# Performance work log

Hardware: AMD Instinct MI355X
Metric: run time of the kernel (lower is better)

The kernel has to match this reference:

```python
import jax, jax.numpy as jnp
import numpy as np

N_NODES = 50000
N_EDGES = 800000
N_GRAPHS = 64


def setup_inputs() -> dict:
    key = jax.random.key(0)
    ks = jax.random.split(key, 13)
    x = jax.random.normal(ks[0], (N_NODES, 1), dtype=jnp.float32)
    edge_index = jax.random.randint(ks[1], (2, N_EDGES), 0, N_NODES)
    batch = jnp.sort(jax.random.randint(ks[2], (N_NODES,), 0, N_GRAPHS))
    def glorot(k, shape):
        fan_in, fan_out = shape
        s = jnp.sqrt(6.0 / (fan_in + fan_out))
        return jax.random.uniform(k, shape, jnp.float32, -s, s)
    W1 = glorot(ks[3], (1, 128));    b1 = jnp.zeros((128,), jnp.float32)
    W2 = glorot(ks[4], (128, 128));  b2 = jnp.zeros((128,), jnp.float32)
    W3 = glorot(ks[5], (128, 256));  b3 = jnp.zeros((256,), jnp.float32)
    Wf1 = glorot(ks[6], (256, 128)); bf1 = jnp.zeros((128,), jnp.float32)
    Wf2 = glorot(ks[7], (128, 10));  bf2 = jnp.zeros((10,), jnp.float32)
    return {"x": x, "edge_index": edge_index, "batch": batch,
            "W1": W1, "b1": b1, "W2": W2, "b2": b2, "W3": W3, "b3": b3,
            "Wf1": Wf1, "bf1": bf1, "Wf2": Wf2, "bf2": bf2}


def _gcn_conv(x, W, b, src, dst, n_nodes):
    # PyG GCNConv: h = X W; out = D^{-1/2} (A + I) D^{-1/2} h + b
    h = x @ W                                  # [N, F_out]
    loop = jnp.arange(n_nodes)
    s = jnp.concatenate([src, loop])           # sources incl. self-loops
    d = jnp.concatenate([dst, loop])           # targets incl. self-loops
    deg = jax.ops.segment_sum(jnp.ones_like(d, h.dtype), d, num_segments=n_nodes)
    dis = jax.lax.rsqrt(jnp.maximum(deg, 1e-12))  # deg >= 1 due to self-loops
    norm = dis[s] * dis[d]                     # [E+N]
    out = jax.ops.segment_sum(h[s] * norm[:, None], d, num_segments=n_nodes)
    return out + b


def reference(x, edge_index, batch, W1, b1, W2, b2, W3, b3, Wf1, bf1, Wf2, bf2):
    src, dst = edge_index[0], edge_index[1]
    n = x.shape[0]
    h = jax.nn.relu(_gcn_conv(x, W1, b1, src, dst, n))
    h = jax.nn.relu(_gcn_conv(h, W2, b2, src, dst, n))
    h = jax.nn.relu(_gcn_conv(h, W3, b3, src, dst, n))   # [N, 256]
    g = jax.ops.segment_max(h, batch, num_segments=N_GRAPHS)  # global_max_pool [G, 256]
    g = jax.nn.relu(g @ Wf1 + bf1)
    # F.dropout with training=self.training: identity in eval mode
    g = g @ Wf2 + bf2
    return jax.nn.relu(g)                       # [G, 10]
```

## Files before the change

### kernel.cpp

```cpp
#include <hip/hip_runtime.h>
#include <hip/hip_bf16.h>

#define N_GRAPHS 64

typedef float f32x4 __attribute__((ext_vector_type(4)));
typedef short bf16x8 __attribute__((ext_vector_type(8)));

__device__ inline unsigned short f2bf(float f) {
    unsigned int u = __float_as_uint(f);
    u = u + 0x7fffu + ((u >> 16) & 1u);
    return (unsigned short)(u >> 16);
}
__device__ inline float bf2f(unsigned short h) {
    return __uint_as_float(((unsigned int)h) << 16);
}

__global__ void k_deg(const int* __restrict__ dst, int E, int* __restrict__ deg) {
    int i = blockIdx.x * blockDim.x + threadIdx.x;
    if (i < E) atomicAdd(&deg[dst[i]], 1);
}

__global__ void k_dis_bsum(const int* __restrict__ deg, const float* __restrict__ x,
                           float* __restrict__ dis, float* __restrict__ xp,
                           int* __restrict__ bsum, int N) {
    int i = blockIdx.x * 256 + threadIdx.x;
    int dv = (i < N) ? deg[i] : 0;
    if (i < N) {
        float d = rsqrtf((float)(dv + 1));
        dis[i] = d;
        xp[i]  = d * x[i];
    }
    int v = dv;
#pragma unroll
    for (int o = 1; o < 64; o <<= 1) v += __shfl_xor(v, o);
    __shared__ int ws4[4];
    if ((threadIdx.x & 63) == 0) ws4[threadIdx.x >> 6] = v;
    __syncthreads();
    if (threadIdx.x == 0) bsum[blockIdx.x] = ws4[0] + ws4[1] + ws4[2] + ws4[3];
}

__device__ inline int block_scan_inc(int v, int* wsum) {
    int lane = threadIdx.x & 63, w = threadIdx.x >> 6;
    int iv = v;
#pragma unroll
    for (int o = 1; o < 64; o <<= 1) {
        int t = __shfl_up(iv, o);
        if (lane >= o) iv += t;
    }
    if (lane == 63) wsum[w] = iv;
    __syncthreads();
    int add = 0;
    for (int k = 0; k < w; ++k) add += wsum[k];
    return iv + add;
}

__global__ void k_scan_sums(const int* __restrict__ bsum, int nb, int* __restrict__ boff) {
    __shared__ int wsum[4];
    int tid = threadIdx.x;
    int v = (tid < nb) ? bsum[tid] : 0;
    int inc = block_scan_inc(v, wsum);
    if (tid < nb) boff[tid] = inc - v;
}

__global__ void k_scan_apply(const int* __restrict__ deg, const int* __restrict__ boff,
                             int* __restrict__ row_ptr, int N) {
    __shared__ int wsum[4];
    int b = blockIdx.x, i = b * 256 + threadIdx.x;
    int v = (i < N) ? deg[i] : 0;
    int inc = block_scan_inc(v, wsum) + boff[b];
    if (i < N) {
        row_ptr[i] = inc - v;
        if (i == N - 1) row_ptr[N] = inc;
    }
}

__global__ void k_scatter(const int* __restrict__ src, const int* __restrict__ dst, int E,
                          const int* __restrict__ row_ptr, int* __restrict__ fill,
                          int* __restrict__ csr_src) {
    int e = blockIdx.x * blockDim.x + threadIdx.x;
    if (e < E) {
        int d = dst[e];
        int pos = row_ptr[d] + atomicAdd(&fill[d], 1);
        csr_src[pos] = src[e];
    }
}

__global__ void k_agg_scalar(const float* __restrict__ xp, const float* __restrict__ dis,
                             const int* __restrict__ row_ptr, const int* __restrict__ csr,
                             float2* __restrict__ td2, int N) {
    int d = blockIdx.x * blockDim.x + threadIdx.x;
    if (d >= N) return;
    float acc = xp[d];
    int e0 = row_ptr[d], e1 = row_ptr[d + 1];
    int e = e0;
    for (; e + 8 <= e1; e += 8) {
        int s0 = csr[e],     s1 = csr[e + 1], s2 = csr[e + 2], s3 = csr[e + 3];
        int s4 = csr[e + 4], s5 = csr[e + 5], s6 = csr[e + 6], s7 = csr[e + 7];
        acc += ((xp[s0] + xp[s1]) + (xp[s2] + xp[s3]))
             + ((xp[s4] + xp[s5]) + (xp[s6] + xp[s7]));
    }
    for (; e < e1; ++e) acc += xp[csr[e]];
    float dd = dis[d];
    td2[d] = make_float2(dd * acc, dd);
}

__global__ void k_h1agg(const float2* __restrict__ td2,
                        const float4* __restrict__ W1f4, const float4* __restrict__ b1f4,
                        const int* __restrict__ row_ptr, const int* __restrict__ csr,
                        float4* __restrict__ out4, int N) {
    int node = blockIdx.x * 8 + (threadIdx.x >> 5);
    int lane = threadIdx.x & 31;
    if (node >= N) return;
    const float4 w1 = W1f4[lane];
    const float4 bv = b1f4[lane];
    float2 sv = td2[node];
    float dd = sv.y;
    float a0 = dd * fmaxf(fmaf(sv.x, w1.x, bv.x), 0.f);
    float a1 = dd * fmaxf(fmaf(sv.x, w1.y, bv.y), 0.f);
    float a2 = dd * fmaxf(fmaf(sv.x, w1.z, bv.z), 0.f);
    float a3 = dd * fmaxf(fmaf(sv.x, w1.w, bv.w), 0.f);
    int e0 = row_ptr[node], e1 = row_ptr[node + 1];
    int e = e0;
    for (; e + 8 <= e1; e += 8) {
        int s0 = csr[e],     s1 = csr[e + 1], s2 = csr[e + 2], s3 = csr[e + 3];
        int s4 = csr[e + 4], s5 = csr[e + 5], s6 = csr[e + 6], s7 = csr[e + 7];
        float2 v0 = td2[s0], v1 = td2[s1], v2 = td2[s2], v3 = td2[s3];
        float2 v4 = td2[s4], v5 = td2[s5], v6 = td2[s6], v7 = td2[s7];
        a0 += ((v0.y * fmaxf(fmaf(v0.x, w1.x, bv.x), 0.f)
              + v1.y * fmaxf(fmaf(v1.x, w1.x, bv.x), 0.f))
             + (v2.y * fmaxf(fmaf(v2.x, w1.x, bv.x), 0.f)
              + v3.y * fmaxf(fmaf(v3.x, w1.x, bv.x), 0.f)))
            + ((v4.y * fmaxf(fmaf(v4.x, w1.x, bv.x), 0.f)
              + v5.y * fmaxf(fmaf(v5.x, w1.x, bv.x), 0.f))
             + (v6.y * fmaxf(fmaf(v6.x, w1.x, bv.x), 0.f)
              + v7.y * fmaxf(fmaf(v7.x, w1.x, bv.x), 0.f)));
        a1 += ((v0.y * fmaxf(fmaf(v0.x, w1.y, bv.y), 0.f)
              + v1.y * fmaxf(fmaf(v1.x, w1.y, bv.y), 0.f))
             + (v2.y * fmaxf(fmaf(v2.x, w1.y, bv.y), 0.f)
              + v3.y * fmaxf(fmaf(v3.x, w1.y, bv.y), 0.f)))
            + ((v4.y * fmaxf(fmaf(v4.x, w1.y, bv.y), 0.f)
              + v5.y * fmaxf(fmaf(v5.x, w1.y, bv.y), 0.f))
             + (v6.y * fmaxf(fmaf(v6.x, w1.y, bv.y), 0.f)
              + v7.y * fmaxf(fmaf(v7.x, w1.y, bv.y), 0.f)));
        a2 += ((v0.y * fmaxf(fmaf(v0.x, w1.z, bv.z), 0.f)
              + v1.y * fmaxf(fmaf(v1.x, w1.z, bv.z), 0.f))
             + (v2.y * fmaxf(fmaf(v2.x, w1.z, bv.z), 0.f)
              + v3.y * fmaxf(fmaf(v3.x, w1.z, bv.z), 0.f)))
            + ((v4.y * fmaxf(fmaf(v4.x, w1.z, bv.z), 0.f)
              + v5.y * fmaxf(fmaf(v5.x, w1.z, bv.z), 0.f))
             + (v6.y * fmaxf(fmaf(v6.x, w1.z, bv.z), 0.f)
              + v7.y * fmaxf(fmaf(v7.x, w1.z, bv.z), 0.f)));
        a3 += ((v0.y * fmaxf(fmaf(v0.x, w1.w, bv.w), 0.f)
              + v1.y * fmaxf(fmaf(v1.x, w1.w, bv.w), 0.f))
             + (v2.y * fmaxf(fmaf(v2.x, w1.w, bv.w), 0.f)
              + v3.y * fmaxf(fmaf(v3.x, w1.w, bv.w), 0.f)))
            + ((v4.y * fmaxf(fmaf(v4.x, w1.w, bv.w), 0.f)
              + v5.y * fmaxf(fmaf(v5.x, w1.w, bv.w), 0.f))
             + (v6.y * fmaxf(fmaf(v6.x, w1.w, bv.w), 0.f)
              + v7.y * fmaxf(fmaf(v7.x, w1.w, bv.w), 0.f)));
    }
    for (; e < e1; ++e) {
        float2 v = td2[csr[e]];
        a0 += v.y * fmaxf(fmaf(v.x, w1.x, bv.x), 0.f);
        a1 += v.y * fmaxf(fmaf(v.x, w1.y, bv.y), 0.f);
        a2 += v.y * fmaxf(fmaf(v.x, w1.z, bv.z), 0.f);
        a3 += v.y * fmaxf(fmaf(v.x, w1.w, bv.w), 0.f);
    }
    out4[(size_t)node * 32 + lane] = make_float4(a0 * dd, a1 * dd, a2 * dd, a3 * dd);
}

__global__ void k_agg128(const float4* __restrict__ hp4, const float* __restrict__ dis,
                         const int* __restrict__ row_ptr, const int* __restrict__ csr,
                         float4* __restrict__ out4, int N) {
    int node = blockIdx.x * 8 + (threadIdx.x >> 5);
    int lane = threadIdx.x & 31;
    if (node >= N) return;
    float4 self = hp4[(size_t)node * 32 + lane];
    float a0 = self.x, a1 = self.y, a2 = self.z, a3 = self.w;
    int e0 = row_ptr[node], e1 = row_ptr[node + 1];
    int e = e0;
    for (; e + 8 <= e1; e += 8) {
        int s0 = csr[e],     s1 = csr[e + 1], s2 = csr[e + 2], s3 = csr[e + 3];
        int s4 = csr[e + 4], s5 = csr[e + 5], s6 = csr[e + 6], s7 = csr[e + 7];
        float4 v0 = hp4[(size_t)s0 * 32 + lane];
        float4 v1 = hp4[(size_t)s1 * 32 + lane];
        float4 v2 = hp4[(size_t)s2 * 32 + lane];
        float4 v3 = hp4[(size_t)s3 * 32 + lane];
        float4 v4 = hp4[(size_t)s4 * 32 + lane];
        float4 v5 = hp4[(size_t)s5 * 32 + lane];
        float4 v6 = hp4[(size_t)s6 * 32 + lane];
        float4 v7 = hp4[(size_t)s7 * 32 + lane];
        a0 += ((v0.x + v1.x) + (v2.x + v3.x)) + ((v4.x + v5.x) + (v6.x + v7.x));
        a1 += ((v0.y + v1.y) + (v2.y + v3.y)) + ((v4.y + v5.y) + (v6.y + v7.y));
        a2 += ((v0.z + v1.z) + (v2.z + v3.z)) + ((v4.z + v5.z) + (v6.z + v7.z));
        a3 += ((v0.w + v1.w) + (v2.w + v3.w)) + ((v4.w + v5.w) + (v6.w + v7.w));
    }
    for (; e < e1; ++e) {
        int s = csr[e];
        float4 v = hp4[(size_t)s * 32 + lane];
        a0 += v.x; a1 += v.y; a2 += v.z; a3 += v.w;
    }
    float d = dis[node];
    out4[(size_t)node * 32 + lane] = make_float4(a0 * d, a1 * d, a2 * d, a3 * d);
}

__global__ void k_wpack(const float* __restrict__ W, int K, int F,
                        unsigned short* __restrict__ WpH,
                        unsigned short* __restrict__ WpL) {
    int idx = blockIdx.x * 256 + threadIdx.x;
    if (idx >= K * F) return;
    int k = idx / F, col = idx - k * F;
    float v = W[idx];
    unsigned short h = f2bf(v);
    unsigned short l = f2bf(v - bf2f(h));
    int o = ((k >> 3) * F + col) * 8 + (k & 7);
    WpH[o] = h; WpL[o] = l;
}

template<int FOUT, bool SCALE, bool FUSE_MAX>
__global__ __launch_bounds__(256, 3) void k_gemm_mfma(
        const float* __restrict__ A,
        const unsigned short* __restrict__ WpH, const unsigned short* __restrict__ WpL,
        const float* __restrict__ b, const float* __restrict__ dis,
        float* __restrict__ outp, const int* __restrict__ batch,
        unsigned int* __restrict__ gmax, int N) {
    __shared__ __align__(16) unsigned short ApH[4 * 4 * 16 * 8];
    __shared__ __align__(16) unsigned short ApL[4 * 4 * 16 * 8];
    __shared__ __align__(16) unsigned short WlH[4 * 128 * 8];
    __shared__ __align__(16) unsigned short WlL[4 * 128 * 8];
    const int tid  = threadIdx.x;
    const int lane = tid & 63;
    const int w    = tid >> 6;
    const int n0   = blockIdx.x * 64;
    const int jh   = blockIdx.y;

    f32x4 acc[8];
#pragma unroll
    for (int ct = 0; ct < 8; ++ct) acc[ct] = (f32x4){0.f, 0.f, 0.f, 0.f};

    for (int kc = 0; kc < 128; kc += 32) {
#pragma unroll
        for (int it = 0; it < 2; ++it) {
            int q = tid + it * 256;
            int kg = q >> 7, cq = q & 127;
            int src = ((kc >> 3) + kg) * FOUT + jh * 128 + cq;
            ((f32x4*)WlH)[q] = ((const f32x4*)WpH)[src];
            ((f32x4*)WlL)[q] = ((const f32x4*)WpL)[src];
        }
#pragma unroll
        for (int it = 0; it < 2; ++it) {
            int idx = tid + it * 256;
            int node = idx >> 3, k4 = idx & 7;
            int gn = n0 + node;
            float4 a = (gn < N)
                ? *reinterpret_cast<const float4*>(A + (size_t)gn * 128 + kc + k4 * 4)
                : make_float4(0.f, 0.f, 0.f, 0.f);
            unsigned short h0 = f2bf(a.x), h1 = f2bf(a.y), h2 = f2bf(a.z), h3 = f2bf(a.w);
            unsigned short l0 = f2bf(a.x - bf2f(h0)), l1 = f2bf(a.y - bf2f(h1));
            unsigned short l2 = f2bf(a.z - bf2f(h2)), l3 = f2bf(a.w - bf2f(h3));
            int kg = k4 >> 1, e0 = (k4 & 1) * 4;
            int base = (((node >> 4) * 4 + kg) * 16 + (node & 15)) * 8 + e0;
            *reinterpret_cast<ushort4*>(&ApH[base]) = make_ushort4(h0, h1, h2, h3);
            *reinterpret_cast<ushort4*>(&ApL[base]) = make_ushort4(l0, l1, l2, l3);
        }
        __syncthreads();

        int aidx = (w * 4 + (lane >> 4)) * 16 + (lane & 15);
        bf16x8 aH = ((const bf16x8*)ApH)[aidx];
        bf16x8 aL = ((const bf16x8*)ApL)[aidx];
#pragma unroll
        for (int ct = 0; ct < 8; ++ct) {
            int bidx = (lane >> 4) * 128 + ct * 16 + (lane & 15);
            bf16x8 bH = ((const bf16x8*)WlH)[bidx];
            bf16x8 bL = ((const bf16x8*)WlL)[bidx];
            acc[ct] = __builtin_amdgcn_mfma_f32_16x16x32_bf16(aL, bL, acc[ct], 0, 0, 0);
            acc[ct] = __builtin_amdgcn_mfma_f32_16x16x32_bf16(aL, bH, acc[ct], 0, 0, 0);
            acc[ct] = __builtin_amdgcn_mfma_f32_16x16x32_bf16(aH, bL, acc[ct], 0, 0, 0);
            acc[ct] = __builtin_amdgcn_mfma_f32_16x16x32_bf16(aH, bH, acc[ct], 0, 0, 0);
        }
        __syncthreads();
    }

    const int cl = lane & 15;
    const int r0 = (lane >> 4) * 4;
    float bb[8];
#pragma unroll
    for (int ct = 0; ct < 8; ++ct) bb[ct] = b[jh * 128 + ct * 16 + cl];

    if (!FUSE_MAX) {
#pragma unroll
        for (int r = 0; r < 4; ++r) {
            int node = n0 + w * 16 + r0 + r;
            if (node < N) {
                float dsc = SCALE ? dis[node] : 1.f;
                float* op = outp + (size_t)node * FOUT + jh * 128 + cl;
#pragma unroll
                for (int ct = 0; ct < 8; ++ct) {
                    float v = fmaxf(acc[ct][r] + bb[ct], 0.f);
                    op[ct * 16] = SCALE ? v * dsc : v;
                }
            }
        }
    } else {
        int nbm[4];
#pragma unroll
        for (int r = 0; r < 4; ++r) {
            int node = n0 + w * 16 + r0 + r;
            nbm[r] = (node < N) ? batch[node] : -1;
        }
        int gfirst = batch[n0];
        int glast  = batch[min(n0 + 63, N - 1)];
        for (int gb = gfirst; gb <= glast; ++gb) {
#pragma unroll
            for (int ct = 0; ct < 8; ++ct) {
                float m = 0.f;
#pragma unroll
                for (int r = 0; r < 4; ++r) {
                    float v = fmaxf(acc[ct][r] + bb[ct], 0.f);
                    if (nbm[r] == gb) m = fmaxf(m, v);
                }
                m = fmaxf(m, __shfl_xor(m, 16));
                m = fmaxf(m, __shfl_xor(m, 32));
                if ((lane >> 4) == 0)
                    atomicMax(&gmax[gb * 256 + jh * 128 + ct * 16 + cl],
                              __float_as_uint(m));
            }
        }
    }
}

__global__ void k_mlp(const float* __restrict__ g, const float* __restrict__ Wf1,
                      const float* __restrict__ bf1, const float* __restrict__ Wf2,
                      const float* __restrict__ bf2, float* __restrict__ out) {
    __shared__ float gr[256];
    __shared__ float g1s[128];
    const int gid = blockIdx.x;
    const int tid = threadIdx.x;
    gr[tid] = g[gid * 256 + tid];
    gr[tid + 128] = g[gid * 256 + 128 + tid];
    __syncthreads();
    float acc = bf1[tid];
    for (int k = 0; k < 256; ++k)
        acc = fmaf(gr[k], Wf1[k * 128 + tid], acc);
    g1s[tid] = fmaxf(acc, 0.f);
    __syncthreads();
    if (tid < 10) {
        float a = bf2[tid];
        for (int k = 0; k < 128; ++k)
            a = fmaf(g1s[k], Wf2[k * 10 + tid], a);
        out[gid * 10 + tid] = fmaxf(a, 0.f);
    }
}

extern "C" void kernel_launch(void* const* d_in, const int* in_sizes, int n_in,
                              void* d_out, int out_size, void* d_ws, size_t ws_size,
                              hipStream_t stream) {
    const float* x   = (const float*)d_in[0];
    const int*   ei  = (const int*)d_in[1];
    const int*   bat = (const int*)d_in[2];
    const float* W1  = (const float*)d_in[3];
    const float* b1  = (const float*)d_in[4];
    const float* W2  = (const float*)d_in[5];
    const float* b2  = (const float*)d_in[6];
    const float* W3  = (const float*)d_in[7];
    const float* b3  = (const float*)d_in[8];
    const float* Wf1 = (const float*)d_in[9];
    const float* bf1 = (const float*)d_in[10];
    const float* Wf2 = (const float*)d_in[11];
    const float* bf2 = (const float*)d_in[12];
    float* out = (float*)d_out;

    const int N = in_sizes[0];
    const int E = in_sizes[1] / 2;
    const int* src = ei;
    const int* dst = ei + E;

    char* base = (char*)d_ws;
    size_t off = 0;
    auto carve = [&](size_t bytes) -> char* {
        char* p = base + off;
        off = (off + bytes + 255) & ~(size_t)255;
        return p;
    };
    const int nb = (N + 255) / 256;
    int*    deg     = (int*)   carve((size_t)N * 4);
    int*    fill    = (int*)   carve((size_t)N * 4);
    int*    row_ptr = (int*)   carve((size_t)(N + 1) * 4);
    int*    csr     = (int*)   carve((size_t)E * 4);
    float*  dis     = (float*) carve((size_t)N * 4);
    float*  xp      = (float*) carve((size_t)N * 4);
    float2* td2     = (float2*)carve((size_t)N * 8);
    float*  A2      = (float*) carve((size_t)N * 128 * 4);
    float*  B2      = (float*) carve((size_t)N * 128 * 4);
    float*  A3      = (float*) carve((size_t)N * 128 * 4);
    unsigned int* g = (unsigned int*)carve((size_t)N_GRAPHS * 256 * 4);
    int*    bsum    = (int*)   carve((size_t)nb * 4);
    int*    boff    = (int*)   carve((size_t)nb * 4);
    unsigned short* Wp2H = (unsigned short*)carve((size_t)128 * 128 * 2);
    unsigned short* Wp2L = (unsigned short*)carve((size_t)128 * 128 * 2);
    unsigned short* Wp3H = (unsigned short*)carve((size_t)128 * 256 * 2);
    unsigned short* Wp3L = (unsigned short*)carve((size_t)128 * 256 * 2);
    (void)ws_size; (void)n_in; (void)out_size;

    hipMemsetAsync(deg, 0, (size_t)N * 4, stream);
    hipMemsetAsync(fill, 0, (size_t)N * 4, stream);
    hipMemsetAsync(g, 0, (size_t)N_GRAPHS * 256 * 4, stream);

    int eb = (E + 255) / 256;

    k_deg<<<eb, 256, 0, stream>>>(dst, E, deg);
    k_dis_bsum<<<nb, 256, 0, stream>>>(deg, x, dis, xp, bsum, N);
    k_scan_sums<<<1, 256, 0, stream>>>(bsum, nb, boff);
    k_scan_apply<<<nb, 256, 0, stream>>>(deg, boff, row_ptr, N);
    k_scatter<<<eb, 256, 0, stream>>>(src, dst, E, row_ptr, fill, csr);

    k_wpack<<<(128 * 128 + 255) / 256, 256, 0, stream>>>(W2, 128, 128, Wp2H, Wp2L);
    k_wpack<<<(128 * 256 + 255) / 256, 256, 0, stream>>>(W3, 128, 256, Wp3H, Wp3L);

    k_agg_scalar<<<nb, 256, 0, stream>>>(xp, dis, row_ptr, csr, td2, N);

    const int gx = (N + 63) / 64;
    const int ab = (N + 7) / 8;

    k_h1agg<<<ab, 256, 0, stream>>>(td2, (const float4*)W1, (const float4*)b1,
                                    row_ptr, csr, (float4*)A2, N);
    k_gemm_mfma<128, true, false><<<dim3(gx, 1), 256, 0, stream>>>(
        A2, Wp2H, Wp2L, b2, dis, B2, nullptr, nullptr, N);

    k_agg128<<<ab, 256, 0, stream>>>((const float4*)B2, dis, row_ptr, csr,
                                     (float4*)A3, N);
    k_gemm_mfma<256, false, true><<<dim3(gx, 2), 256, 0, stream>>>(
        A3, Wp3H, Wp3L, b3, nullptr, nullptr, bat, g, N);

    k_mlp<<<N_GRAPHS, 128, 0, stream>>>((const float*)g, Wf1, bf1, Wf2, bf2, out);
}
```

Measured before the change: 250.1 us.

## Split 128-wide aggregation into two column-half passes and merge small launches

The 128-feature neighbour aggregation now runs as two launches, each gathering only one 64-column half of every source row with 16 lanes per node. This halves the gather working set per pass (25.6 MB of the 50000x128 table down to 12.8 MB) so it fits better in cache, and the output is written with nontemporal stores. The cost is reading the CSR index arrays twice and doing two launches. The two weight-packing kernels are also merged into one launch, and two adjacent memsets become a single memset, which assumes the deg and fill buffers are contiguous in the workspace.

```diff
diff --git a/kernel.cpp b/kernel.cpp
--- a/kernel.cpp
+++ b/kernel.cpp
@@ -169,27 +169,28 @@
     out4[(size_t)node * 32 + lane] = make_float4(a0 * dd, a1 * dd, a2 * dd, a3 * dd);
 }
 
-__global__ void k_agg128(const float4* __restrict__ hp4, const float* __restrict__ dis,
-                         const int* __restrict__ row_ptr, const int* __restrict__ csr,
-                         float4* __restrict__ out4, int N) {
-    int node = blockIdx.x * 8 + (threadIdx.x >> 5);
-    int lane = threadIdx.x & 31;
+__global__ void k_agg128h(const float4* __restrict__ hp4, const float* __restrict__ dis,
+                          const int* __restrict__ row_ptr, const int* __restrict__ csr,
+                          float4* __restrict__ out4, int N, int half) {
+    int node = blockIdx.x * 16 + (threadIdx.x >> 4);
+    int lane = threadIdx.x & 15;
     if (node >= N) return;
-    float4 self = hp4[(size_t)node * 32 + lane];
+    const int co = half * 16 + lane;
+    float4 self = hp4[(size_t)node * 32 + co];
     float a0 = self.x, a1 = self.y, a2 = self.z, a3 = self.w;
     int e0 = row_ptr[node], e1 = row_ptr[node + 1];
     int e = e0;
     for (; e + 8 <= e1; e += 8) {
         int s0 = csr[e],     s1 = csr[e + 1], s2 = csr[e + 2], s3 = csr[e + 3];
         int s4 = csr[e + 4], s5 = csr[e + 5], s6 = csr[e + 6], s7 = csr[e + 7];
-        float4 v0 = hp4[(size_t)s0 * 32 + lane];
-        float4 v1 = hp4[(size_t)s1 * 32 + lane];
-        float4 v2 = hp4[(size_t)s2 * 32 + lane];
-        float4 v3 = hp4[(size_t)s3 * 32 + lane];
-        float4 v4 = hp4[(size_t)s4 * 32 + lane];
-        float4 v5 = hp4[(size_t)s5 * 32 + lane];
-        float4 v6 = hp4[(size_t)s6 * 32 + lane];
-        float4 v7 = hp4[(size_t)s7 * 32 + lane];
+        float4 v0 = hp4[(size_t)s0 * 32 + co];
+        float4 v1 = hp4[(size_t)s1 * 32 + co];
+        float4 v2 = hp4[(size_t)s2 * 32 + co];
+        float4 v3 = hp4[(size_t)s3 * 32 + co];
+        float4 v4 = hp4[(size_t)s4 * 32 + co];
+        float4 v5 = hp4[(size_t)s5 * 32 + co];
+        float4 v6 = hp4[(size_t)s6 * 32 + co];
+        float4 v7 = hp4[(size_t)s7 * 32 + co];
         a0 += ((v0.x + v1.x) + (v2.x + v3.x)) + ((v4.x + v5.x) + (v6.x + v7.x));
         a1 += ((v0.y + v1.y) + (v2.y + v3.y)) + ((v4.y + v5.y) + (v6.y + v7.y));
         a2 += ((v0.z + v1.z) + (v2.z + v3.z)) + ((v4.z + v5.z) + (v6.z + v7.z));
@@ -197,20 +198,25 @@
     }
     for (; e < e1; ++e) {
         int s = csr[e];
-        float4 v = hp4[(size_t)s * 32 + lane];
+        float4 v = hp4[(size_t)s * 32 + co];
         a0 += v.x; a1 += v.y; a2 += v.z; a3 += v.w;
     }
     float d = dis[node];
-    out4[(size_t)node * 32 + lane] = make_float4(a0 * d, a1 * d, a2 * d, a3 * d);
-}
-
-__global__ void k_wpack(const float* __restrict__ W, int K, int F,
-                        unsigned short* __restrict__ WpH,
-                        unsigned short* __restrict__ WpL) {
+    f32x4 r = {a0 * d, a1 * d, a2 * d, a3 * d};
+    __builtin_nontemporal_store(r, (f32x4*)&out4[(size_t)node * 32 + co]);
+}
+
+__global__ void k_wpack2(const float* __restrict__ W2, const float* __restrict__ W3,
+                         unsigned short* __restrict__ Wp2H, unsigned short* __restrict__ Wp2L,
+                         unsigned short* __restrict__ Wp3H, unsigned short* __restrict__ Wp3L) {
     int idx = blockIdx.x * 256 + threadIdx.x;
-    if (idx >= K * F) return;
-    int k = idx / F, col = idx - k * F;
-    float v = W[idx];
+    const float* W; unsigned short *WpH, *WpL; int F, j;
+    if (idx < 128 * 128) { W = W2; WpH = Wp2H; WpL = Wp2L; F = 128; j = idx; }
+    else if (idx < 128 * 128 + 128 * 256) {
+        W = W3; WpH = Wp3H; WpL = Wp3L; F = 256; j = idx - 128 * 128;
+    } else return;
+    int k = j / F, col = j - k * F;
+    float v = W[j];
     unsigned short h = f2bf(v);
     unsigned short l = f2bf(v - bf2f(h));
     int o = ((k >> 3) * F + col) * 8 + (k & 7);
@@ -402,8 +408,7 @@
     unsigned short* Wp3L = (unsigned short*)carve((size_t)128 * 256 * 2);
     (void)ws_size; (void)n_in; (void)out_size;
 
-    hipMemsetAsync(deg, 0, (size_t)N * 4, stream);
-    hipMemsetAsync(fill, 0, (size_t)N * 4, stream);
+    hipMemsetAsync(deg, 0, (size_t)((char*)row_ptr - (char*)deg), stream);
     hipMemsetAsync(g, 0, (size_t)N_GRAPHS * 256 * 4, stream);
 
     int eb = (E + 255) / 256;
@@ -414,21 +419,24 @@
     k_scan_apply<<<nb, 256, 0, stream>>>(deg, boff, row_ptr, N);
     k_scatter<<<eb, 256, 0, stream>>>(src, dst, E, row_ptr, fill, csr);
 
-    k_wpack<<<(128 * 128 + 255) / 256, 256, 0, stream>>>(W2, 128, 128, Wp2H, Wp2L);
-    k_wpack<<<(128 * 256 + 255) / 256, 256, 0, stream>>>(W3, 128, 256, Wp3H, Wp3L);
+    k_wpack2<<<(128 * 128 + 128 * 256 + 255) / 256, 256, 0, stream>>>(
+        W2, W3, Wp2H, Wp2L, Wp3H, Wp3L);
 
     k_agg_scalar<<<nb, 256, 0, stream>>>(xp, dis, row_ptr, csr, td2, N);
 
     const int gx = (N + 63) / 64;
     const int ab = (N + 7) / 8;
+    const int ab16 = (N + 15) / 16;
 
     k_h1agg<<<ab, 256, 0, stream>>>(td2, (const float4*)W1, (const float4*)b1,
                                     row_ptr, csr, (float4*)A2, N);
     k_gemm_mfma<128, true, false><<<dim3(gx, 1), 256, 0, stream>>>(
         A2, Wp2H, Wp2L, b2, dis, B2, nullptr, nullptr, N);
 
-    k_agg128<<<ab, 256, 0, stream>>>((const float4*)B2, dis, row_ptr, csr,
-                                     (float4*)A3, N);
+    k_agg128h<<<ab16, 256, 0, stream>>>((const float4*)B2, dis, row_ptr, csr,
+                                        (float4*)A3, N, 0);
+    k_agg128h<<<ab16, 256, 0, stream>>>((const float4*)B2, dis, row_ptr, csr,
+                                        (float4*)A3, N, 1);
     k_gemm_mfma<256, false, true><<<dim3(gx, 2), 256, 0, stream>>>(
         A3, Wp3H, Wp3L, b3, nullptr, nullptr, bat, g, N);
 
```

New measurement: 240.5 us. 1.04x faster.
